# Kernel optimization log

Hardware: AMD Instinct MI355X
Metric: run time of the kernel (lower is better)

Reference implementation:

```python
import jax, jax.numpy as jnp
import numpy as np

BATCH = 16384
NUM_CLASSES = 1000
FEA_DIM = 1024
MARGIN = 5.0


def setup_inputs() -> dict:
    key = jax.random.key(0)
    k1, k2, k3 = jax.random.split(key, 3)
    x = jax.random.normal(k1, (BATCH, FEA_DIM), dtype=jnp.float32)
    labels = jax.random.randint(k2, (BATCH,), 0, NUM_CLASSES)
    centers = jax.random.normal(k3, (NUM_CLASSES, FEA_DIM), dtype=jnp.float32)
    return {"x": x, "labels": labels, "centers": centers}


def reference(x, labels, centers):
    # Half squared euclidean distances via the GEMM expansion:
    # 0.5*||a-b||^2 = 0.5*(||a||^2 + ||b||^2 - 2 a.b)
    B = x.shape[0]
    C = centers.shape[0]
    x2 = jnp.sum(x * x, axis=1, keepdims=True)          # [B,1]
    c2 = jnp.sum(centers * centers, axis=1)             # [C]
    d_xc = 0.5 * (x2 + c2[None, :] - 2.0 * (x @ centers.T))   # [B,C]
    d_cc = 0.5 * (c2[:, None] + c2[None, :] - 2.0 * (centers @ centers.T))  # [C,C]

    is_label = labels[:, None] == jnp.arange(C)[None, :]  # [B,C] bool
    inf = jnp.float32(jnp.inf)

    # pos_center: distance to own class center
    pos = jnp.take_along_axis(d_xc, labels[:, None], axis=1)[:, 0]       # [B]
    # neg_center: min distance to any other class center
    neg = jnp.min(jnp.where(is_label, inf, d_xc), axis=1)                # [B]
    # centers term: min distance between own center and any other center
    cen = jnp.min(jnp.where(is_label, inf, d_cc[labels]), axis=1)        # [B]

    loss = jax.nn.relu(pos + MARGIN - neg) + jax.nn.relu(MARGIN + 2.0 - cen)
    return jnp.sum(loss) / B
```

## Files before the change

kernel.cpp:

```cpp
#include <hip/hip_runtime.h>
#include <hip/hip_bf16.h>
#include <stdint.h>

#define BATCH   16384
#define NCLASS  1000
#define CPAD    1024
#define FDIM    1024
#define MARGINF 5.0f

typedef __attribute__((ext_vector_type(4))) float f32x4;
typedef __attribute__((ext_vector_type(8))) short bf16x8;

__device__ __forceinline__ void gload16(const void* g, void* l) {
    __builtin_amdgcn_global_load_lds(
        (const __attribute__((address_space(1))) void*)g,
        (__attribute__((address_space(3))) void*)l, 16, 0, 0);
}

__device__ __forceinline__ unsigned short f2bf(float f) {
    __hip_bfloat16 h = __float2bfloat16(f);
    return __builtin_bit_cast(unsigned short, h);
}

__global__ void prep_x(const float* __restrict__ x, unsigned short* __restrict__ xb, int n4) {
    int i = blockIdx.x * blockDim.x + threadIdx.x;
    int stride = gridDim.x * blockDim.x;
    for (; i < n4; i += stride) {
        float4 v = ((const float4*)x)[i];
        ushort4 o;
        o.x = f2bf(v.x); o.y = f2bf(v.y); o.z = f2bf(v.z); o.w = f2bf(v.w);
        ((ushort4*)xb)[i] = o;
    }
}

__global__ void prep_c(const float* __restrict__ c, unsigned short* __restrict__ cb,
                       float* __restrict__ c2) {
    int k = blockIdx.x;
    int t = threadIdx.x;
    if (k >= NCLASS) {
        ((ushort4*)(cb + (size_t)k * FDIM))[t] = make_ushort4(0, 0, 0, 0);
        if (t == 0) c2[k] = 1e30f;
        return;
    }
    float4 v = ((const float4*)(c + (size_t)k * FDIM))[t];
    ushort4 o;
    o.x = f2bf(v.x); o.y = f2bf(v.y); o.z = f2bf(v.z); o.w = f2bf(v.w);
    ((ushort4*)(cb + (size_t)k * FDIM))[t] = o;
    float ss = v.x * v.x + v.y * v.y + v.z * v.z + v.w * v.w;
    #pragma unroll
    for (int s = 1; s < 64; s <<= 1) ss += __shfl_xor(ss, s, 64);
    __shared__ float sred[4];
    int lane = t & 63, wid = t >> 6;
    if (lane == 0) sred[wid] = ss;
    __syncthreads();
    if (t == 0) c2[k] = sred[0] + sred[1] + sred[2] + sred[3];
}

template <bool EXROW>
__launch_bounds__(256)
__global__ void gemm_min(const unsigned short* __restrict__ A,
                         const unsigned short* __restrict__ B,
                         const float* __restrict__ c2,
                         const int* __restrict__ labels,
                         float* __restrict__ pmin,
                         float* __restrict__ pos)
{
    constexpr int BM = 128, BK = 64, KTOT = 1024, NCT = 8;
    __shared__ __align__(16) char sA[BM * BK * 2];
    __shared__ __align__(16) char sB[BM * BK * 2];
    __shared__ int   sLab[BM];
    __shared__ float sPM[2 * BM];

    const int t    = threadIdx.x;
    const int lane = t & 63;
    const int wave = t >> 6;
    const int wrow = wave >> 1, wcol = wave & 1;
    const int lo4  = lane & 15, hi2 = lane >> 4;

    const int rowBase = blockIdx.x * BM;
    const int colBase = blockIdx.y * BM;

    if (!EXROW) { if (t < BM) sLab[t] = labels[rowBase + t]; }

    f32x4 acc[4][4];
    #pragma unroll
    for (int m = 0; m < 4; m++)
        #pragma unroll
        for (int n = 0; n < 4; n++) acc[m][n] = (f32x4){0.f, 0.f, 0.f, 0.f};

    const int g_t = t & 7;
    const int r_t = t >> 3;

    for (int kt = 0; kt < KTOT / BK; ++kt) {
        __syncthreads();
        const int k0 = kt * BK;
        #pragma unroll
        for (int cc = 0; cc < 4; ++cc) {
            const int row = cc * 32 + r_t;
            const int sc  = g_t ^ (row & 7);
            const unsigned short* ga = A + (size_t)(rowBase + row) * KTOT + k0 + sc * 8;
            const unsigned short* gb = B + (size_t)(colBase + row) * KTOT + k0 + sc * 8;
            char* la = sA + (cc * 256 + (t & 192)) * 16;
            char* lb = sB + (cc * 256 + (t & 192)) * 16;
            gload16(ga, la);
            gload16(gb, lb);
        }
        __syncthreads();
        #pragma unroll
        for (int ks = 0; ks < 2; ++ks) {
            bf16x8 af[4], bfr[4];
            #pragma unroll
            for (int m = 0; m < 4; m++) {
                const int r    = wrow * 64 + m * 16 + lo4;
                const int slot = (ks * 4 + hi2) ^ (r & 7);
                af[m] = *(const bf16x8*)(sA + r * 128 + slot * 16);
            }
            #pragma unroll
            for (int n = 0; n < 4; n++) {
                const int r    = wcol * 64 + n * 16 + lo4;
                const int slot = (ks * 4 + hi2) ^ (r & 7);
                bfr[n] = *(const bf16x8*)(sB + r * 128 + slot * 16);
            }
            #pragma unroll
            for (int m = 0; m < 4; m++)
                #pragma unroll
                for (int n = 0; n < 4; n++)
                    acc[m][n] = __builtin_amdgcn_mfma_f32_16x16x32_bf16(af[m], bfr[n], acc[m][n], 0, 0, 0);
        }
    }

    float bias[4]; int colg[4];
    #pragma unroll
    for (int n = 0; n < 4; n++) {
        const int col = colBase + wcol * 64 + n * 16 + lo4;
        colg[n] = col;
        bias[n] = 0.5f * c2[col];
    }
    #pragma unroll
    for (int m = 0; m < 4; m++) {
        #pragma unroll
        for (int j = 0; j < 4; j++) {
            const int rloc  = wrow * 64 + m * 16 + hi2 * 4 + j;
            const int rglob = rowBase + rloc;
            const int lab   = EXROW ? rglob : sLab[rloc];
            float vmin = 1e30f;
            #pragma unroll
            for (int n = 0; n < 4; n++) {
                float tv = acc[m][n][j] + bias[n];
                if (colg[n] == lab) {
                    if (!EXROW) pos[rglob] = tv;
                    tv = 1e30f;
                }
                vmin = fminf(vmin, tv);
            }
            vmin = fminf(vmin, __shfl_xor(vmin, 1, 64));
            vmin = fminf(vmin, __shfl_xor(vmin, 2, 64));
            vmin = fminf(vmin, __shfl_xor(vmin, 4, 64));
            vmin = fminf(vmin, __shfl_xor(vmin, 8, 64));
            if (lo4 == 0) sPM[wcol * BM + rloc] = vmin;
        }
    }
    __syncthreads();
    if (t < BM) {
        const float v = fminf(sPM[t], sPM[BM + t]);
        pmin[(size_t)(rowBase + t) * NCT + blockIdx.y] = v;
    }
}

__global__ void cmin_k(const float* __restrict__ c2, const float* __restrict__ cpmin,
                       float* __restrict__ cmin) {
    int k = blockIdx.x * blockDim.x + threadIdx.x;
    if (k >= NCLASS) return;
    float v = 1e30f;
    #pragma unroll
    for (int i = 0; i < 8; i++) v = fminf(v, cpmin[k * 8 + i]);
    cmin[k] = 0.5f * c2[k] + v;
}

__global__ void loss_k(const float* __restrict__ pmin, const float* __restrict__ pos,
                       const int* __restrict__ labels, const float* __restrict__ cmin,
                       float* __restrict__ partial) {
    int r = blockIdx.x * 256 + threadIdx.x;
    float neg = 1e30f;
    #pragma unroll
    for (int i = 0; i < 8; i++) neg = fminf(neg, pmin[(size_t)r * 8 + i]);
    float l1 = fmaxf(pos[r] + MARGINF - neg, 0.f);
    float l2 = fmaxf(MARGINF + 2.0f - cmin[labels[r]], 0.f);
    float v  = l1 + l2;
    #pragma unroll
    for (int s = 1; s < 64; s <<= 1) v += __shfl_xor(v, s, 64);
    __shared__ float sred[4];
    int lane = threadIdx.x & 63, wid = threadIdx.x >> 6;
    if (lane == 0) sred[wid] = v;
    __syncthreads();
    if (threadIdx.x == 0) partial[blockIdx.x] = sred[0] + sred[1] + sred[2] + sred[3];
}

__global__ void sum_k(const float* __restrict__ partial, float* __restrict__ out) {
    float v = partial[threadIdx.x];
    #pragma unroll
    for (int s = 1; s < 64; s <<= 1) v += __shfl_xor(v, s, 64);
    if (threadIdx.x == 0) out[0] = v / (float)BATCH;
}

extern "C" void kernel_launch(void* const* d_in, const int* in_sizes, int n_in,
                              void* d_out, int out_size, void* d_ws, size_t ws_size,
                              hipStream_t stream) {
    const float* x       = (const float*)d_in[0];
    const int*   labels  = (const int*)d_in[1];
    const float* centers = (const float*)d_in[2];
    float* out = (float*)d_out;

    char* ws = (char*)d_ws;
    size_t off = 0;
    unsigned short* xb = (unsigned short*)(ws + off); off += (size_t)BATCH * FDIM * 2;
    unsigned short* cb = (unsigned short*)(ws + off); off += (size_t)CPAD * FDIM * 2;
    float* c2      = (float*)(ws + off); off += (size_t)CPAD * 4;
    float* pmin    = (float*)(ws + off); off += (size_t)BATCH * 8 * 4;
    float* pos     = (float*)(ws + off); off += (size_t)BATCH * 4;
    float* cpmin   = (float*)(ws + off); off += (size_t)CPAD * 8 * 4;
    float* cmin    = (float*)(ws + off); off += (size_t)CPAD * 4;
    float* partial = (float*)(ws + off); off += 64 * 4;

    prep_x<<<dim3(2048), dim3(256), 0, stream>>>(x, xb, BATCH * FDIM / 4);
    prep_c<<<dim3(CPAD), dim3(256), 0, stream>>>(centers, cb, c2);
    gemm_min<false><<<dim3(BATCH / 128, 8), dim3(256), 0, stream>>>(xb, cb, c2, labels, pmin, pos);
    gemm_min<true><<<dim3(CPAD / 128, 8), dim3(256), 0, stream>>>(cb, cb, c2, nullptr, cpmin, nullptr);
    cmin_k<<<dim3(4), dim3(256), 0, stream>>>(c2, cpmin, cmin);
    loss_k<<<dim3(BATCH / 256), dim3(256), 0, stream>>>(pmin, pos, labels, cmin, partial);
    sum_k<<<dim3(1), dim3(64), 0, stream>>>(partial, out);
}
```

Baseline: 175.5 us.

## Merge prep, GEMM and reduction kernels to cut launch count

Fuses the x and centers conversion into one prep kernel and runs the x-centers and centers-centers GEMMs as a single launch over a flat block index. It also folds the cmin and final-sum kernels into loss_k, which now uses an atomic add after a memset. Label lookup moves from shared memory to a direct global load, the reduction scratch reuses sA, and launch bounds request 5 blocks per CU. The aim is to remove launch gaps and tail serialization between small kernels, at the cost of a float atomic whose summation order is nondeterministic.

```diff
diff --git a/kernel.cpp b/kernel.cpp
--- a/kernel.cpp
+++ b/kernel.cpp
@@ -22,54 +22,63 @@
     return __builtin_bit_cast(unsigned short, h);
 }
 
-__global__ void prep_x(const float* __restrict__ x, unsigned short* __restrict__ xb, int n4) {
-    int i = blockIdx.x * blockDim.x + threadIdx.x;
-    int stride = gridDim.x * blockDim.x;
-    for (; i < n4; i += stride) {
-        float4 v = ((const float4*)x)[i];
+__global__ void prep(const float* __restrict__ x, const float* __restrict__ c,
+                     unsigned short* __restrict__ xb, unsigned short* __restrict__ cb,
+                     float* __restrict__ c2) {
+    const int bid = blockIdx.x;
+    const int t   = threadIdx.x;
+    if (bid < CPAD) {
+        const int k = bid;
+        if (k >= NCLASS) {
+            ((ushort4*)(cb + (size_t)k * FDIM))[t] = make_ushort4(0, 0, 0, 0);
+            if (t == 0) c2[k] = 1e30f;
+            return;
+        }
+        float4 v = ((const float4*)(c + (size_t)k * FDIM))[t];
         ushort4 o;
         o.x = f2bf(v.x); o.y = f2bf(v.y); o.z = f2bf(v.z); o.w = f2bf(v.w);
-        ((ushort4*)xb)[i] = o;
-    }
-}
-
-__global__ void prep_c(const float* __restrict__ c, unsigned short* __restrict__ cb,
-                       float* __restrict__ c2) {
-    int k = blockIdx.x;
-    int t = threadIdx.x;
-    if (k >= NCLASS) {
-        ((ushort4*)(cb + (size_t)k * FDIM))[t] = make_ushort4(0, 0, 0, 0);
-        if (t == 0) c2[k] = 1e30f;
-        return;
-    }
-    float4 v = ((const float4*)(c + (size_t)k * FDIM))[t];
-    ushort4 o;
-    o.x = f2bf(v.x); o.y = f2bf(v.y); o.z = f2bf(v.z); o.w = f2bf(v.w);
-    ((ushort4*)(cb + (size_t)k * FDIM))[t] = o;
-    float ss = v.x * v.x + v.y * v.y + v.z * v.z + v.w * v.w;
-    #pragma unroll
-    for (int s = 1; s < 64; s <<= 1) ss += __shfl_xor(ss, s, 64);
-    __shared__ float sred[4];
-    int lane = t & 63, wid = t >> 6;
-    if (lane == 0) sred[wid] = ss;
-    __syncthreads();
-    if (t == 0) c2[k] = sred[0] + sred[1] + sred[2] + sred[3];
-}
-
-template <bool EXROW>
-__launch_bounds__(256)
-__global__ void gemm_min(const unsigned short* __restrict__ A,
-                         const unsigned short* __restrict__ B,
+        ((ushort4*)(cb + (size_t)k * FDIM))[t] = o;
+        float ss = v.x * v.x + v.y * v.y + v.z * v.z + v.w * v.w;
+        #pragma unroll
+        for (int s = 1; s < 64; s <<= 1) ss += __shfl_xor(ss, s, 64);
+        __shared__ float sred[4];
+        int lane = t & 63, wid = t >> 6;
+        if (lane == 0) sred[wid] = ss;
+        __syncthreads();
+        if (t == 0) c2[k] = sred[0] + sred[1] + sred[2] + sred[3];
+    } else {
+        const int n4 = BATCH * FDIM / 4;
+        int i = (bid - CPAD) * 256 + t;
+        const int stride = 2048 * 256;
+        #pragma unroll
+        for (int it = 0; it < 8; ++it, i += stride) {
+            if (i < n4) {
+                float4 v = ((const float4*)x)[i];
+                ushort4 o;
+                o.x = f2bf(v.x); o.y = f2bf(v.y); o.z = f2bf(v.z); o.w = f2bf(v.w);
+                ((ushort4*)xb)[i] = o;
+            }
+        }
+    }
+}
+
+__launch_bounds__(256, 5)
+__global__ void gemm_min(const unsigned short* __restrict__ xb,
+                         const unsigned short* __restrict__ cb,
                          const float* __restrict__ c2,
                          const int* __restrict__ labels,
                          float* __restrict__ pmin,
+                         float* __restrict__ cpmin,
                          float* __restrict__ pos)
 {
     constexpr int BM = 128, BK = 64, KTOT = 1024, NCT = 8;
     __shared__ __align__(16) char sA[BM * BK * 2];
     __shared__ __align__(16) char sB[BM * BK * 2];
-    __shared__ int   sLab[BM];
-    __shared__ float sPM[2 * BM];
+
+    const int bid  = blockIdx.x;
+    const bool cc  = (bid >= 1024);
+    const int bx   = cc ? (bid - 1024) & 7 : bid & 127;
+    const int by   = cc ? (bid - 1024) >> 3 : bid >> 7;
 
     const int t    = threadIdx.x;
     const int lane = t & 63;
@@ -77,10 +86,10 @@
     const int wrow = wave >> 1, wcol = wave & 1;
     const int lo4  = lane & 15, hi2 = lane >> 4;
 
-    const int rowBase = blockIdx.x * BM;
-    const int colBase = blockIdx.y * BM;
-
-    if (!EXROW) { if (t < BM) sLab[t] = labels[rowBase + t]; }
+    const int rowBase = bx * BM;
+    const int colBase = by * BM;
+    const unsigned short* A = cc ? cb : xb;
+    float* pout = cc ? cpmin : pmin;
 
     f32x4 acc[4][4];
     #pragma unroll
@@ -95,13 +104,13 @@
         __syncthreads();
         const int k0 = kt * BK;
         #pragma unroll
-        for (int cc = 0; cc < 4; ++cc) {
-            const int row = cc * 32 + r_t;
+        for (int cch = 0; cch < 4; ++cch) {
+            const int row = cch * 32 + r_t;
             const int sc  = g_t ^ (row & 7);
-            const unsigned short* ga = A + (size_t)(rowBase + row) * KTOT + k0 + sc * 8;
-            const unsigned short* gb = B + (size_t)(colBase + row) * KTOT + k0 + sc * 8;
-            char* la = sA + (cc * 256 + (t & 192)) * 16;
-            char* lb = sB + (cc * 256 + (t & 192)) * 16;
+            const unsigned short* ga = A  + (size_t)(rowBase + row) * KTOT + k0 + sc * 8;
+            const unsigned short* gb = cb + (size_t)(colBase + row) * KTOT + k0 + sc * 8;
+            char* la = sA + (cch * 256 + (t & 192)) * 16;
+            char* lb = sB + (cch * 256 + (t & 192)) * 16;
             gload16(ga, la);
             gload16(gb, lb);
         }
@@ -129,6 +138,9 @@
         }
     }
 
+    __syncthreads();
+    float* sPM = (float*)sA;
+
     float bias[4]; int colg[4];
     #pragma unroll
     for (int n = 0; n < 4; n++) {
@@ -142,13 +154,13 @@
         for (int j = 0; j < 4; j++) {
             const int rloc  = wrow * 64 + m * 16 + hi2 * 4 + j;
             const int rglob = rowBase + rloc;
-            const int lab   = EXROW ? rglob : sLab[rloc];
+            const int lab   = cc ? rglob : labels[rglob];
             float vmin = 1e30f;
             #pragma unroll
             for (int n = 0; n < 4; n++) {
                 float tv = acc[m][n][j] + bias[n];
                 if (colg[n] == lab) {
-                    if (!EXROW) pos[rglob] = tv;
+                    if (!cc) pos[rglob] = tv;
                     tv = 1e30f;
                 }
                 vmin = fminf(vmin, tv);
@@ -163,44 +175,31 @@
     __syncthreads();
     if (t < BM) {
         const float v = fminf(sPM[t], sPM[BM + t]);
-        pmin[(size_t)(rowBase + t) * NCT + blockIdx.y] = v;
-    }
-}
-
-__global__ void cmin_k(const float* __restrict__ c2, const float* __restrict__ cpmin,
-                       float* __restrict__ cmin) {
-    int k = blockIdx.x * blockDim.x + threadIdx.x;
-    if (k >= NCLASS) return;
-    float v = 1e30f;
-    #pragma unroll
-    for (int i = 0; i < 8; i++) v = fminf(v, cpmin[k * 8 + i]);
-    cmin[k] = 0.5f * c2[k] + v;
+        pout[(size_t)(rowBase + t) * NCT + by] = v;
+    }
 }
 
 __global__ void loss_k(const float* __restrict__ pmin, const float* __restrict__ pos,
-                       const int* __restrict__ labels, const float* __restrict__ cmin,
-                       float* __restrict__ partial) {
-    int r = blockIdx.x * 256 + threadIdx.x;
+                       const int* __restrict__ labels, const float* __restrict__ cpmin,
+                       const float* __restrict__ c2, float* __restrict__ out) {
+    const int r = blockIdx.x * 256 + threadIdx.x;
     float neg = 1e30f;
     #pragma unroll
     for (int i = 0; i < 8; i++) neg = fminf(neg, pmin[(size_t)r * 8 + i]);
-    float l1 = fmaxf(pos[r] + MARGINF - neg, 0.f);
-    float l2 = fmaxf(MARGINF + 2.0f - cmin[labels[r]], 0.f);
-    float v  = l1 + l2;
+    const int lab = labels[r];
+    float cmin = 1e30f;
+    #pragma unroll
+    for (int i = 0; i < 8; i++) cmin = fminf(cmin, cpmin[(size_t)lab * 8 + i]);
+    const float cen = 0.5f * c2[lab] + cmin;
+    float v = fmaxf(pos[r] + MARGINF - neg, 0.f) + fmaxf(MARGINF + 2.0f - cen, 0.f);
     #pragma unroll
     for (int s = 1; s < 64; s <<= 1) v += __shfl_xor(v, s, 64);
     __shared__ float sred[4];
     int lane = threadIdx.x & 63, wid = threadIdx.x >> 6;
     if (lane == 0) sred[wid] = v;
     __syncthreads();
-    if (threadIdx.x == 0) partial[blockIdx.x] = sred[0] + sred[1] + sred[2] + sred[3];
-}
-
-__global__ void sum_k(const float* __restrict__ partial, float* __restrict__ out) {
-    float v = partial[threadIdx.x];
-    #pragma unroll
-    for (int s = 1; s < 64; s <<= 1) v += __shfl_xor(v, s, 64);
-    if (threadIdx.x == 0) out[0] = v / (float)BATCH;
+    if (threadIdx.x == 0)
+        atomicAdd(out, (sred[0] + sred[1] + sred[2] + sred[3]) * (1.0f / (float)BATCH));
 }
 
 extern "C" void kernel_launch(void* const* d_in, const int* in_sizes, int n_in,
@@ -215,18 +214,13 @@
     size_t off = 0;
     unsigned short* xb = (unsigned short*)(ws + off); off += (size_t)BATCH * FDIM * 2;
     unsigned short* cb = (unsigned short*)(ws + off); off += (size_t)CPAD * FDIM * 2;
-    float* c2      = (float*)(ws + off); off += (size_t)CPAD * 4;
-    float* pmin    = (float*)(ws + off); off += (size_t)BATCH * 8 * 4;
-    float* pos     = (float*)(ws + off); off += (size_t)BATCH * 4;
-    float* cpmin   = (float*)(ws + off); off += (size_t)CPAD * 8 * 4;
-    float* cmin    = (float*)(ws + off); off += (size_t)CPAD * 4;
-    float* partial = (float*)(ws + off); off += 64 * 4;
-
-    prep_x<<<dim3(2048), dim3(256), 0, stream>>>(x, xb, BATCH * FDIM / 4);
-    prep_c<<<dim3(CPAD), dim3(256), 0, stream>>>(centers, cb, c2);
-    gemm_min<false><<<dim3(BATCH / 128, 8), dim3(256), 0, stream>>>(xb, cb, c2, labels, pmin, pos);
-    gemm_min<true><<<dim3(CPAD / 128, 8), dim3(256), 0, stream>>>(cb, cb, c2, nullptr, cpmin, nullptr);
-    cmin_k<<<dim3(4), dim3(256), 0, stream>>>(c2, cpmin, cmin);
-    loss_k<<<dim3(BATCH / 256), dim3(256), 0, stream>>>(pmin, pos, labels, cmin, partial);
-    sum_k<<<dim3(1), dim3(64), 0, stream>>>(partial, out);
-}
+    float* c2    = (float*)(ws + off); off += (size_t)CPAD * 4;
+    float* pmin  = (float*)(ws + off); off += (size_t)BATCH * 8 * 4;
+    float* pos   = (float*)(ws + off); off += (size_t)BATCH * 4;
+    float* cpmin = (float*)(ws + off); off += (size_t)CPAD * 8 * 4;
+
+    hipMemsetAsync(out, 0, sizeof(float), stream);
+    prep<<<dim3(CPAD + 2048), dim3(256), 0, stream>>>(x, centers, xb, cb, c2);
+    gemm_min<<<dim3(1024 + 64), dim3(256), 0, stream>>>(xb, cb, c2, labels, pmin, cpmin, pos);
+    loss_k<<<dim3(BATCH / 256), dim3(256), 0, stream>>>(pmin, pos, labels, cpmin, c2, out);
+}
```

New measurement: 192.1 us. 9.4% more time.
